# Kernel tuning notes

Hardware: AMD Instinct MI355X
Metric: run time of the kernel (lower is better)

Reference implementation:

```python
import jax, jax.numpy as jnp
import numpy as np

T = 2048         # seq_len (nbatch in original code)
IN = 384         # input_size (npts)
H = 2 * IN       # hidden_dim = 768
NL = 10          # n_layers
NOUT = 384       # output_size


def setup_inputs() -> dict:
    key = jax.random.key(0)
    ks = jax.random.split(key, 12)
    s_in = 1.0 / np.sqrt(H)  # PyTorch GRU init scale
    inp = {
        "x": jax.random.normal(ks[0], (T, IN), dtype=jnp.float32),
        # layer 0 (input_size -> H)
        "w_ih0": jax.random.uniform(ks[1], (3 * H, IN), jnp.float32, -s_in, s_in),
        "w_hh0": jax.random.uniform(ks[2], (3 * H, H), jnp.float32, -s_in, s_in),
        "b_ih0": jax.random.uniform(ks[3], (3 * H,), jnp.float32, -s_in, s_in),
        "b_hh0": jax.random.uniform(ks[4], (3 * H,), jnp.float32, -s_in, s_in),
        # layers 1..9 (H -> H), stacked
        "w_ih": jax.random.uniform(ks[5], (NL - 1, 3 * H, H), jnp.float32, -s_in, s_in),
        "w_hh": jax.random.uniform(ks[6], (NL - 1, 3 * H, H), jnp.float32, -s_in, s_in),
        "b_ih": jax.random.uniform(ks[7], (NL - 1, 3 * H), jnp.float32, -s_in, s_in),
        "b_hh": jax.random.uniform(ks[8], (NL - 1, 3 * H), jnp.float32, -s_in, s_in),
        # final linear head
        "fc_w": jax.random.uniform(ks[9], (NOUT, H), jnp.float32, -s_in, s_in),
        "fc_b": jax.random.uniform(ks[10], (NOUT,), jnp.float32, -s_in, s_in),
    }
    return inp


def _gru_layer(xs, w_ih, w_hh, b_ih, b_hh):
    # xs: [T, D_in] -> ys: [T, H]. PyTorch GRU cell semantics.
    gi = xs @ w_ih.T + b_ih          # [T, 3H] input projections, batched GEMM up front

    def step(h, gi_t):
        gh = h @ w_hh.T + b_hh       # [3H]
        i_r, i_z, i_n = jnp.split(gi_t, 3)
        h_r, h_z, h_n = jnp.split(gh, 3)
        r = jax.nn.sigmoid(i_r + h_r)
        z = jax.nn.sigmoid(i_z + h_z)
        n = jnp.tanh(i_n + r * h_n)
        h_new = (1.0 - z) * n + z * h
        return h_new, h_new

    h0 = jnp.zeros((xs.shape[1] if False else w_hh.shape[1],), xs.dtype)  # [H]
    _, ys = jax.lax.scan(step, h0, gi)
    return ys


def reference(x, w_ih0, w_hh0, b_ih0, b_hh0, w_ih, w_hh, b_ih, b_hh, fc_w, fc_b):
    # batch_size = 1 in the original; hidden initialized to zeros each call.
    h = _gru_layer(x, w_ih0, w_hh0, b_ih0, b_hh0)   # layer 0
    for l in range(NL - 1):                           # layers 1..9 (fixed small loop)
        h = _gru_layer(h, w_ih[l], w_hh[l], b_ih[l], b_hh[l])
    out = h @ fc_w.T + fc_b                           # [T, NOUT]
    return out
```

## Files before the change

kernel.cpp:

```cpp
#include <hip/hip_runtime.h>


#define T_SEQ 2048
#define H_DIM 768
#define IN0   384
#define G3    2304
#define NLAYER 10
#define BPL   24
#define NBLK  (NLAYER * BPL)
#define UPB   32
#define NTHR  512
#define NOUT  384
#define CTR_STRIDE 32
#define RING  16
#define WIH_STRIDE 776
#define HCS_STRIDE 52
#define HSD_STRIDE 56
#define HSD0_STRIDE 32

typedef _Float16 half2_t __attribute__((ext_vector_type(2)));
typedef _Float16 half8_t __attribute__((ext_vector_type(8)));
typedef unsigned long long u64;

__device__ __forceinline__ float sigm(float x) { return 1.0f / (1.0f + __expf(-x)); }

__device__ __forceinline__ u64 ld64(const u64* p) {
    return __hip_atomic_load(p, __ATOMIC_RELAXED, __HIP_MEMORY_SCOPE_AGENT);
}
__device__ __forceinline__ void st64(u64* p, u64 v) {
    __hip_atomic_store(p, v, __ATOMIC_RELAXED, __HIP_MEMORY_SCOPE_AGENT);
}
__device__ __forceinline__ unsigned ldctr(const unsigned* p) {
    return __hip_atomic_load(p, __ATOMIC_RELAXED, __HIP_MEMORY_SCOPE_AGENT);
}
__device__ __forceinline__ unsigned tag_of(u64 u) { return (unsigned)(u >> 32); }
__device__ __forceinline__ float    val_of(u64 u) { return __uint_as_float((unsigned)u); }
__device__ __forceinline__ u64      pack(float v, unsigned t) {
    return ((u64)t << 32) | (u64)__float_as_uint(v);
}

__device__ __forceinline__ float dot8(half8_t h, half8_t w, float acc) {
    union U { half8_t v; unsigned u[4]; };
    U H; H.v = h; U W; W.v = w;
#pragma unroll
    for (int j = 0; j < 4; ++j) {
#if __has_builtin(__builtin_amdgcn_fdot2)
        acc = __builtin_amdgcn_fdot2(__builtin_bit_cast(half2_t, H.u[j]),
                                     __builtin_bit_cast(half2_t, W.u[j]), acc, false);
#else
        half2_t a = __builtin_bit_cast(half2_t, H.u[j]);
        half2_t b = __builtin_bit_cast(half2_t, W.u[j]);
        asm volatile("v_dot2_f32_f16 %0, %1, %2, %0" : "+v"(acc) : "v"(a), "v"(b));
#endif
    }
    return acc;
}

extern "C" __global__ __launch_bounds__(NTHR, 1) void gru_flow(
    const float* __restrict__ x,
    const float* __restrict__ wih0,
    const float* __restrict__ whh0,
    const float* __restrict__ bih0,
    const float* __restrict__ bhh0,
    const float* __restrict__ wihS,
    const float* __restrict__ whhS,
    const float* __restrict__ bihS,
    const float* __restrict__ bhhS,
    u64* __restrict__ ring64,
    float* __restrict__ h9,
    unsigned int* __restrict__ ctr)
{
    __shared__ _Float16 wih16[96 * WIH_STRIDE];
    __shared__ float    hcs[16 * HCS_STRIDE];
    __shared__ _Float16 hsd16[16 * HSD_STRIDE];

    const int tid  = threadIdx.x;
    const int lane = tid & 63;
    const int wv   = tid >> 6;
    const int p    = lane & 15;
    const int ulocal = wv * 4 + (lane >> 4);
    const int bid  = blockIdx.x;
    const int layer = bid / BPL;
    const int sub   = bid % BPL;
    const int uglob = sub * UPB + ulocal;
    const int Din   = layer ? H_DIM : IN0;

    const float* wihL = layer ? wihS + (size_t)(layer - 1) * G3 * H_DIM : wih0;
    const float* whhL = layer ? whhS + (size_t)(layer - 1) * G3 * H_DIM : whh0;
    const float* bihL = layer ? bihS + (size_t)(layer - 1) * G3 : bih0;
    const float* bhhL = layer ? bhhS + (size_t)(layer - 1) * G3 : bhh0;

    float4 wr[3][12];
#pragma unroll
    for (int gate = 0; gate < 3; ++gate) {
        const float4* src = (const float4*)(whhL + (size_t)(uglob + gate * H_DIM) * H_DIM + 48 * p);
#pragma unroll
        for (int i = 0; i < 12; ++i) wr[gate][i] = src[i];
    }
    const float bhr  = bhhL[uglob], bhz = bhhL[uglob + H_DIM], bhn  = bhhL[uglob + 2 * H_DIM];
    const float bir  = bihL[uglob], biz = bihL[uglob + H_DIM], bin_ = bihL[uglob + 2 * H_DIM];

    for (int rr = 0; rr < 12; ++rr) {
        const int r = wv * 12 + rr;
        const int u = r / 3, G = r % 3;
        const float* src = wihL + (size_t)(sub * UPB + u + G * H_DIM) * Din;
        _Float16* dst = wih16 + r * WIH_STRIDE;
        for (int k = lane; k < Din; k += 64) dst[k] = (_Float16)src[k];
    }
    __syncthreads();

    float gi_r = 0.f, gi_z = 0.f, gi_n = 0.f;
    auto ih_gemv = [&]() {
        float sr = 0.f, sz = 0.f, sn = 0.f;
        if (layer) {
            const half8_t* h8 = (const half8_t*)(hsd16 + p * HSD_STRIDE);
            const half8_t* w0 = (const half8_t*)(wih16 + (ulocal * 3 + 0) * WIH_STRIDE + 48 * p);
            const half8_t* w1 = (const half8_t*)(wih16 + (ulocal * 3 + 1) * WIH_STRIDE + 48 * p);
            const half8_t* w2 = (const half8_t*)(wih16 + (ulocal * 3 + 2) * WIH_STRIDE + 48 * p);
#pragma unroll
            for (int i = 0; i < 6; ++i) {
                const half8_t hv = h8[i];
                sr = dot8(hv, w0[i], sr);
                sz = dot8(hv, w1[i], sz);
                sn = dot8(hv, w2[i], sn);
            }
        } else {
            const half8_t* h8 = (const half8_t*)(hsd16 + p * HSD0_STRIDE);
            const half8_t* w0 = (const half8_t*)(wih16 + (ulocal * 3 + 0) * WIH_STRIDE + 24 * p);
            const half8_t* w1 = (const half8_t*)(wih16 + (ulocal * 3 + 1) * WIH_STRIDE + 24 * p);
            const half8_t* w2 = (const half8_t*)(wih16 + (ulocal * 3 + 2) * WIH_STRIDE + 24 * p);
#pragma unroll
            for (int i = 0; i < 3; ++i) {
                const half8_t hv = h8[i];
                sr = dot8(hv, w0[i], sr);
                sz = dot8(hv, w1[i], sz);
                sn = dot8(hv, w2[i], sn);
            }
        }
#pragma unroll
        for (int off = 1; off <= 8; off <<= 1) {
            sr += __shfl_xor(sr, off, 64);
            sz += __shfl_xor(sz, off, 64);
            sn += __shfl_xor(sn, off, 64);
        }
        gi_r = sr + bir; gi_z = sz + biz; gi_n = sn + bin_;
    };

    if (layer) {
        const u64* sr_ = ring64 + (size_t)(layer - 1) * RING * H_DIM;
        for (;;) {
            const u64 a = ld64(sr_ + tid);
            int ok = (tag_of(a) == 1u);
            hsd16[(tid / 48) * HSD_STRIDE + tid % 48] = (_Float16)val_of(a);
            if (tid < 256) {
                const u64 b = ld64(sr_ + tid + 512);
                ok &= (tag_of(b) == 1u);
                hsd16[((tid + 512) / 48) * HSD_STRIDE + (tid + 512) % 48] = (_Float16)val_of(b);
            }
            if (__syncthreads_and(ok)) break;
            __builtin_amdgcn_s_sleep(1);
        }
    } else {
        if (tid < IN0) hsd16[(tid / 24) * HSD0_STRIDE + tid % 24] = (_Float16)x[tid];
        __syncthreads();
    }
    ih_gemv();

    unsigned bp = 0;
    u64 sh0 = 0, sh1 = 0;
    float xsh = 0.f;

    for (int t = 0; t < T_SEQ; ++t) {
        if (layer != NLAYER - 1 && t >= 16 && (t & 3) == 0) {
            const unsigned tgt = 24u * (unsigned)((t - 12) >> 2);
            while (bp < tgt) {
                __builtin_amdgcn_s_sleep(2);
                bp = ldctr(&ctr[(layer + 1) * CTR_STRIDE]);
            }
        }

        const int tn = t + 1;

        if (tn < T_SEQ) {
            if (layer) {
                const u64* sr_ = ring64 + ((size_t)(layer - 1) * RING + (tn & (RING - 1))) * H_DIM;
                sh0 = ld64(sr_ + tid);
                if (tid < 256) sh1 = ld64(sr_ + tid + 512);
            } else if (tid < IN0) {
                xsh = x[(size_t)tn * IN0 + tid];
            }
        }

        if (t > 0) {
            const u64* hr = ring64 + ((size_t)layer * RING + ((t - 1) & (RING - 1))) * H_DIM;
            for (;;) {
                const u64 a = ld64(hr + tid);
                int ok = (tag_of(a) == (unsigned)t);
                hcs[(tid / 48) * HCS_STRIDE + tid % 48] = val_of(a);
                if (tid < 256) {
                    const u64 b = ld64(hr + tid + 512);
                    ok &= (tag_of(b) == (unsigned)t);
                    hcs[((tid + 512) / 48) * HCS_STRIDE + (tid + 512) % 48] = val_of(b);
                }
                if (__syncthreads_and(ok)) break;
            }
        } else {
            __syncthreads();
        }

        float ar = 0.f, az = 0.f, an = 0.f;
        if (t > 0) {
            const float4* hs = (const float4*)(hcs + p * HCS_STRIDE);
#pragma unroll
            for (int i = 0; i < 12; ++i) {
                const float4 h4 = hs[i];
                ar += h4.x * wr[0][i].x + h4.y * wr[0][i].y + h4.z * wr[0][i].z + h4.w * wr[0][i].w;
                az += h4.x * wr[1][i].x + h4.y * wr[1][i].y + h4.z * wr[1][i].z + h4.w * wr[1][i].w;
                an += h4.x * wr[2][i].x + h4.y * wr[2][i].y + h4.z * wr[2][i].z + h4.w * wr[2][i].w;
            }
        }
#pragma unroll
        for (int off = 1; off <= 8; off <<= 1) {
            ar += __shfl_xor(ar, off, 64);
            az += __shfl_xor(az, off, 64);
            an += __shfl_xor(an, off, 64);
        }
        if (p == 0) {
            const float hp = (t > 0) ? hcs[(uglob / 48) * HCS_STRIDE + uglob % 48] : 0.f;
            const float r = sigm(ar + bhr + gi_r);
            const float z = sigm(az + bhz + gi_z);
            const float n = tanhf(gi_n + r * (an + bhn));
            const float hnew = (1.f - z) * n + z * hp;
            st64(&ring64[((size_t)layer * RING + (t & (RING - 1))) * H_DIM + uglob],
                 pack(hnew, (unsigned)(t + 1)));
            if (layer == NLAYER - 1) h9[(size_t)t * H_DIM + uglob] = hnew;
        }

        if (tn < T_SEQ) {
            if (layer) {
                for (;;) {
                    int ok = (tag_of(sh0) == (unsigned)(tn + 1));
                    hsd16[(tid / 48) * HSD_STRIDE + tid % 48] = (_Float16)val_of(sh0);
                    if (tid < 256) {
                        ok &= (tag_of(sh1) == (unsigned)(tn + 1));
                        hsd16[((tid + 512) / 48) * HSD_STRIDE + (tid + 512) % 48] = (_Float16)val_of(sh1);
                    }
                    if (__syncthreads_and(ok)) break;
                    const u64* sr_ = ring64 + ((size_t)(layer - 1) * RING + (tn & (RING - 1))) * H_DIM;
                    sh0 = ld64(sr_ + tid);
                    if (tid < 256) sh1 = ld64(sr_ + tid + 512);
                }
            } else {
                if (tid < IN0) hsd16[(tid / 24) * HSD0_STRIDE + tid % 24] = (_Float16)xsh;
                __syncthreads();
            }
            ih_gemv();
        }

        if ((t & 3) == 3) {
            if (tid == 0 && layer)
                __hip_atomic_fetch_add(&ctr[layer * CTR_STRIDE], 1u,
                                       __ATOMIC_RELAXED, __HIP_MEMORY_SCOPE_AGENT);
            if (layer != NLAYER - 1)
                bp = ldctr(&ctr[(layer + 1) * CTR_STRIDE]);
        }
    }
}

extern "C" __global__ __launch_bounds__(NOUT, 1) void fc_head(
    const float* __restrict__ h,
    const float* __restrict__ fw,
    const float* __restrict__ fb,
    float* __restrict__ out)
{
    __shared__ float hs[H_DIM];
    const int t = blockIdx.x;
    const float* hr = h + (size_t)t * H_DIM;
    for (int k = threadIdx.x; k < H_DIM; k += NOUT) hs[k] = hr[k];
    __syncthreads();

    const int o = threadIdx.x;
    const float4* wr4 = (const float4*)(fw + (size_t)o * H_DIM);
    const float4* hs4 = (const float4*)hs;
    float acc = fb[o];
#pragma unroll 8
    for (int k = 0; k < H_DIM / 4; ++k) {
        const float4 w = wr4[k], hv = hs4[k];
        acc += w.x * hv.x + w.y * hv.y + w.z * hv.z + w.w * hv.w;
    }
    out[(size_t)t * NOUT + o] = acc;
}

extern "C" void kernel_launch(void* const* d_in, const int* in_sizes, int n_in,
                              void* d_out, int out_size, void* d_ws, size_t ws_size,
                              hipStream_t stream)
{
    const float* x    = (const float*)d_in[0];
    const float* wih0 = (const float*)d_in[1];
    const float* whh0 = (const float*)d_in[2];
    const float* bih0 = (const float*)d_in[3];
    const float* bhh0 = (const float*)d_in[4];
    const float* wihS = (const float*)d_in[5];
    const float* whhS = (const float*)d_in[6];
    const float* bihS = (const float*)d_in[7];
    const float* bhhS = (const float*)d_in[8];
    const float* fcw  = (const float*)d_in[9];
    const float* fcb  = (const float*)d_in[10];

    char* ws = (char*)d_ws;
    unsigned int* ctr = (unsigned int*)ws;
    u64* ring64 = (u64*)(ws + 65536);
    float* h9   = (float*)(ws + 65536 + (size_t)NLAYER * RING * H_DIM * 8);

    hipMemsetAsync(ctr, 0, 65536, stream);
    hipMemsetAsync(ring64, 0, (size_t)NLAYER * RING * H_DIM * 8, stream);

    hipLaunchKernelGGL(gru_flow, dim3(NBLK), dim3(NTHR), 0, stream,
                       x, wih0, whh0, bih0, bhh0, wihS, whhS, bihS, bhhS,
                       ring64, h9, ctr);

    hipLaunchKernelGGL(fc_head, dim3(T_SEQ), dim3(NOUT), 0, stream,
                       h9, fcw, fcb, (float*)d_out);
}
```

Baseline: 7.689 ms.

## Double-buffer LDS state and replace block-wide spin barriers with per-thread polling

Each thread now spins on its own ring entries until the expected tag appears, instead of the whole block retrying via __syncthreads_and loops. The hidden-state and input staging buffers in shared memory are double-buffered, so one __syncthreads per step suffices. Next-step ring loads are issued early, right after the state update. This cuts the barrier count per timestep on the serial recurrence path, at the cost of more shared memory and per-thread busy polling.

```diff
diff --git a/kernel.cpp b/kernel.cpp
--- a/kernel.cpp
+++ b/kernel.cpp
@@ -70,9 +70,9 @@
     float* __restrict__ h9,
     unsigned int* __restrict__ ctr)
 {
-    __shared__ _Float16 wih16[96 * WIH_STRIDE];
-    __shared__ float    hcs[16 * HCS_STRIDE];
-    __shared__ _Float16 hsd16[16 * HSD_STRIDE];
+    __shared__ __align__(16) _Float16 wih16[96 * WIH_STRIDE];
+    __shared__ __align__(16) float    hcs[2][16 * HCS_STRIDE];
+    __shared__ __align__(16) _Float16 hsd16[2][16 * HSD_STRIDE];
 
     const int tid  = threadIdx.x;
     const int lane = tid & 63;
@@ -84,6 +84,7 @@
     const int sub   = bid % BPL;
     const int uglob = sub * UPB + ulocal;
     const int Din   = layer ? H_DIM : IN0;
+    const bool w2   = (tid < 256);
 
     const float* wihL = layer ? wihS + (size_t)(layer - 1) * G3 * H_DIM : wih0;
     const float* whhL = layer ? whhS + (size_t)(layer - 1) * G3 * H_DIM : whh0;
@@ -110,31 +111,31 @@
     __syncthreads();
 
     float gi_r = 0.f, gi_z = 0.f, gi_n = 0.f;
-    auto ih_gemv = [&]() {
+    auto ih_gemv = [&](int b) {
         float sr = 0.f, sz = 0.f, sn = 0.f;
         if (layer) {
-            const half8_t* h8 = (const half8_t*)(hsd16 + p * HSD_STRIDE);
+            const half8_t* h8 = (const half8_t*)(&hsd16[b][p * HSD_STRIDE]);
             const half8_t* w0 = (const half8_t*)(wih16 + (ulocal * 3 + 0) * WIH_STRIDE + 48 * p);
             const half8_t* w1 = (const half8_t*)(wih16 + (ulocal * 3 + 1) * WIH_STRIDE + 48 * p);
-            const half8_t* w2 = (const half8_t*)(wih16 + (ulocal * 3 + 2) * WIH_STRIDE + 48 * p);
+            const half8_t* wn = (const half8_t*)(wih16 + (ulocal * 3 + 2) * WIH_STRIDE + 48 * p);
 #pragma unroll
             for (int i = 0; i < 6; ++i) {
                 const half8_t hv = h8[i];
                 sr = dot8(hv, w0[i], sr);
                 sz = dot8(hv, w1[i], sz);
-                sn = dot8(hv, w2[i], sn);
+                sn = dot8(hv, wn[i], sn);
             }
         } else {
-            const half8_t* h8 = (const half8_t*)(hsd16 + p * HSD0_STRIDE);
+            const half8_t* h8 = (const half8_t*)(&hsd16[b][p * HSD0_STRIDE]);
             const half8_t* w0 = (const half8_t*)(wih16 + (ulocal * 3 + 0) * WIH_STRIDE + 24 * p);
             const half8_t* w1 = (const half8_t*)(wih16 + (ulocal * 3 + 1) * WIH_STRIDE + 24 * p);
-            const half8_t* w2 = (const half8_t*)(wih16 + (ulocal * 3 + 2) * WIH_STRIDE + 24 * p);
+            const half8_t* wn = (const half8_t*)(wih16 + (ulocal * 3 + 2) * WIH_STRIDE + 24 * p);
 #pragma unroll
             for (int i = 0; i < 3; ++i) {
                 const half8_t hv = h8[i];
                 sr = dot8(hv, w0[i], sr);
                 sz = dot8(hv, w1[i], sz);
-                sn = dot8(hv, w2[i], sn);
+                sn = dot8(hv, wn[i], sn);
             }
         }
 #pragma unroll
@@ -147,30 +148,37 @@
     };
 
     if (layer) {
-        const u64* sr_ = ring64 + (size_t)(layer - 1) * RING * H_DIM;
-        for (;;) {
-            const u64 a = ld64(sr_ + tid);
-            int ok = (tag_of(a) == 1u);
-            hsd16[(tid / 48) * HSD_STRIDE + tid % 48] = (_Float16)val_of(a);
-            if (tid < 256) {
-                const u64 b = ld64(sr_ + tid + 512);
-                ok &= (tag_of(b) == 1u);
-                hsd16[((tid + 512) / 48) * HSD_STRIDE + (tid + 512) % 48] = (_Float16)val_of(b);
-            }
-            if (__syncthreads_and(ok)) break;
-            __builtin_amdgcn_s_sleep(1);
+        const u64* sp = ring64 + (size_t)(layer - 1) * RING * H_DIM;
+        u64 a = ld64(sp + tid);
+        while (tag_of(a) != 1u) a = ld64(sp + tid);
+        hsd16[1][(tid / 48) * HSD_STRIDE + tid % 48] = (_Float16)val_of(a);
+        if (w2) {
+            u64 c = ld64(sp + tid + 512);
+            while (tag_of(c) != 1u) c = ld64(sp + tid + 512);
+            hsd16[1][((tid + 512) / 48) * HSD_STRIDE + (tid + 512) % 48] = (_Float16)val_of(c);
         }
     } else {
-        if (tid < IN0) hsd16[(tid / 24) * HSD0_STRIDE + tid % 24] = (_Float16)x[tid];
-        __syncthreads();
-    }
-    ih_gemv();
+        if (tid < IN0) hsd16[1][(tid / 24) * HSD0_STRIDE + tid % 24] = (_Float16)x[tid];
+    }
+    __syncthreads();
+    ih_gemv(1);
+
+    u64 ca0 = 0, ca1 = 0, sa0 = 0, sa1 = 0;
+    float xs = 0.f;
+    if (layer) {
+        const u64* sp = ring64 + ((size_t)(layer - 1) * RING + 1) * H_DIM;
+        sa0 = ld64(sp + tid);
+        if (w2) sa1 = ld64(sp + tid + 512);
+    } else if (tid < IN0) {
+        xs = x[IN0 + tid];
+    }
 
     unsigned bp = 0;
-    u64 sh0 = 0, sh1 = 0;
-    float xsh = 0.f;
 
     for (int t = 0; t < T_SEQ; ++t) {
+        const int b = t & 1;
+        const bool have_s = (t + 1) < T_SEQ;
+
         if (layer != NLAYER - 1 && t >= 16 && (t & 3) == 0) {
             const unsigned tgt = 24u * (unsigned)((t - 12) >> 2);
             while (bp < tgt) {
@@ -179,38 +187,35 @@
             }
         }
 
-        const int tn = t + 1;
-
-        if (tn < T_SEQ) {
-            if (layer) {
-                const u64* sr_ = ring64 + ((size_t)(layer - 1) * RING + (tn & (RING - 1))) * H_DIM;
-                sh0 = ld64(sr_ + tid);
-                if (tid < 256) sh1 = ld64(sr_ + tid + 512);
-            } else if (tid < IN0) {
-                xsh = x[(size_t)tn * IN0 + tid];
-            }
-        }
-
         if (t > 0) {
             const u64* hr = ring64 + ((size_t)layer * RING + ((t - 1) & (RING - 1))) * H_DIM;
-            for (;;) {
-                const u64 a = ld64(hr + tid);
-                int ok = (tag_of(a) == (unsigned)t);
-                hcs[(tid / 48) * HCS_STRIDE + tid % 48] = val_of(a);
-                if (tid < 256) {
-                    const u64 b = ld64(hr + tid + 512);
-                    ok &= (tag_of(b) == (unsigned)t);
-                    hcs[((tid + 512) / 48) * HCS_STRIDE + (tid + 512) % 48] = val_of(b);
+            while (tag_of(ca0) != (unsigned)t) ca0 = ld64(hr + tid);
+            hcs[b][(tid / 48) * HCS_STRIDE + tid % 48] = val_of(ca0);
+            if (w2) {
+                while (tag_of(ca1) != (unsigned)t) ca1 = ld64(hr + tid + 512);
+                hcs[b][((tid + 512) / 48) * HCS_STRIDE + (tid + 512) % 48] = val_of(ca1);
+            }
+        }
+
+        if (have_s) {
+            if (layer) {
+                const u64* sp = ring64 + ((size_t)(layer - 1) * RING + ((t + 1) & (RING - 1))) * H_DIM;
+                while (tag_of(sa0) != (unsigned)(t + 2)) sa0 = ld64(sp + tid);
+                hsd16[b][(tid / 48) * HSD_STRIDE + tid % 48] = (_Float16)val_of(sa0);
+                if (w2) {
+                    while (tag_of(sa1) != (unsigned)(t + 2)) sa1 = ld64(sp + tid + 512);
+                    hsd16[b][((tid + 512) / 48) * HSD_STRIDE + (tid + 512) % 48] = (_Float16)val_of(sa1);
                 }
-                if (__syncthreads_and(ok)) break;
-            }
-        } else {
-            __syncthreads();
-        }
+            } else {
+                if (tid < IN0) hsd16[b][(tid / 24) * HSD0_STRIDE + tid % 24] = (_Float16)xs;
+            }
+        }
+
+        __syncthreads();
 
         float ar = 0.f, az = 0.f, an = 0.f;
         if (t > 0) {
-            const float4* hs = (const float4*)(hcs + p * HCS_STRIDE);
+            const float4* hs = (const float4*)(&hcs[b][p * HCS_STRIDE]);
 #pragma unroll
             for (int i = 0; i < 12; ++i) {
                 const float4 h4 = hs[i];
@@ -226,7 +231,7 @@
             an += __shfl_xor(an, off, 64);
         }
         if (p == 0) {
-            const float hp = (t > 0) ? hcs[(uglob / 48) * HCS_STRIDE + uglob % 48] : 0.f;
+            const float hp = (t > 0) ? hcs[b][(uglob / 48) * HCS_STRIDE + uglob % 48] : 0.f;
             const float r = sigm(ar + bhr + gi_r);
             const float z = sigm(az + bhz + gi_z);
             const float n = tanhf(gi_n + r * (an + bhn));
@@ -236,26 +241,22 @@
             if (layer == NLAYER - 1) h9[(size_t)t * H_DIM + uglob] = hnew;
         }
 
-        if (tn < T_SEQ) {
-            if (layer) {
-                for (;;) {
-                    int ok = (tag_of(sh0) == (unsigned)(tn + 1));
-                    hsd16[(tid / 48) * HSD_STRIDE + tid % 48] = (_Float16)val_of(sh0);
-                    if (tid < 256) {
-                        ok &= (tag_of(sh1) == (unsigned)(tn + 1));
-                        hsd16[((tid + 512) / 48) * HSD_STRIDE + (tid + 512) % 48] = (_Float16)val_of(sh1);
-                    }
-                    if (__syncthreads_and(ok)) break;
-                    const u64* sr_ = ring64 + ((size_t)(layer - 1) * RING + (tn & (RING - 1))) * H_DIM;
-                    sh0 = ld64(sr_ + tid);
-                    if (tid < 256) sh1 = ld64(sr_ + tid + 512);
+        if (have_s) {
+            const u64* hrn = ring64 + ((size_t)layer * RING + (t & (RING - 1))) * H_DIM;
+            ca0 = ld64(hrn + tid);
+            if (w2) ca1 = ld64(hrn + tid + 512);
+            if ((t + 2) < T_SEQ) {
+                if (layer) {
+                    const u64* spn = ring64 + ((size_t)(layer - 1) * RING + ((t + 2) & (RING - 1))) * H_DIM;
+                    sa0 = ld64(spn + tid);
+                    if (w2) sa1 = ld64(spn + tid + 512);
+                } else if (tid < IN0) {
+                    xs = x[(size_t)(t + 2) * IN0 + tid];
                 }
-            } else {
-                if (tid < IN0) hsd16[(tid / 24) * HSD0_STRIDE + tid % 24] = (_Float16)xsh;
-                __syncthreads();
-            }
-            ih_gemv();
-        }
+            }
+        }
+
+        if (have_s) ih_gemv(b);
 
         if ((t & 3) == 3) {
             if (tid == 0 && layer)
```

Measured after the change: 7.000 ms. -9.0%, faster.
